# Kernel tuning notes

Measured on AMD Instinct MI355X. Metric: run time of the kernel, lower is better.

The kernel has to match this reference:

```python
import jax, jax.numpy as jnp
import numpy as np

SPECIAL = 4  # special_word_num

def _lstm_cell(x, h, c, Wih, Whh, b):
    # torch gate order: i, f, g, o ; gates = x@Wih.T + h@Whh.T + b
    g = x @ Wih.T + h @ Whh.T + b
    i, f, gg, o = jnp.split(g, 4, axis=-1)
    c_new = jax.nn.sigmoid(f) * c + jax.nn.sigmoid(i) * jnp.tanh(gg)
    h_new = jax.nn.sigmoid(o) * jnp.tanh(c_new)
    return h_new, c_new

def _lstm_scan(xs, h0, c0, Wih, Whh, b):
    def step(carry, x):
        h, c = carry
        h, c = _lstm_cell(x, h, c, Wih, Whh, b)
        return (h, c), h
    (hT, cT), hs = jax.lax.scan(step, (h0, c0), xs)
    return hs, hT, cT  # hs: [T, B, H]

def _forward(article, art_lens, tar_len, emb, enc_Wih_f, enc_Whh_f, enc_b_f,
             enc_Wih_b, enc_Whh_b, enc_b_b, init_enc_h, init_enc_c,
             dec_hW, dec_cW, attn_wm, attn_wq, proj_W1, proj_b1, proj_W2,
             dec_Wih, dec_Whh, dec_b):
    Tsrc, B, _ = article.shape
    H = init_enc_h.shape[1]
    # ---- encoder: 1-layer bidirectional LSTM with learned init states ----
    h0f = jnp.broadcast_to(init_enc_h[0], (B, H)); c0f = jnp.broadcast_to(init_enc_c[0], (B, H))
    h0b = jnp.broadcast_to(init_enc_h[1], (B, H)); c0b = jnp.broadcast_to(init_enc_c[1], (B, H))
    out_f, hTf, cTf = _lstm_scan(article, h0f, c0f, enc_Wih_f, enc_Whh_f, enc_b_f)
    out_b, hTb, cTb = _lstm_scan(article[::-1], h0b, c0b, enc_Wih_b, enc_Whh_b, enc_b_b)
    enc_art = jnp.concatenate([out_f, out_b[::-1]], axis=-1)  # [T, B, 2H]
    final_h = jnp.concatenate([hTf, hTb], axis=-1)  # [B, 2H]
    final_c = jnp.concatenate([cTf, cTb], axis=-1)
    init_h = final_h @ dec_hW  # [B, H]
    init_c = final_c @ dec_cW
    # ---- attention memory + mask ----
    attention = jnp.einsum('tbe,eh->bth', enc_art, attn_wm)  # [B, T, H]
    mask = jnp.arange(Tsrc)[None, :] < art_lens[:, None]      # [B, T]
    lens = art_lens.astype(attention.dtype)[:, None]
    seq_mean = jnp.sum(attention * mask[:, :, None], axis=1) / lens  # [B, H]
    def project(x):
        return jnp.tanh(x @ proj_W1 + proj_b1) @ proj_W2
    init_out = project(jnp.concatenate([init_h, seq_mean], axis=1))  # [B, H/2]
    # ---- sequential decoder over tar_len steps (lax.scan) ----
    embs = emb[SPECIAL + jnp.arange(tar_len)]  # [Ttgt, E]
    NEG = jnp.asarray(-1e9, attention.dtype)
    def dec_step(carry, emb_i):
        h, c, prev_out = carry
        x = jnp.concatenate([jnp.broadcast_to(emb_i, (B, emb_i.shape[0])), prev_out], axis=1)
        h, c = _lstm_cell(x, h, c, dec_Wih, dec_Whh, dec_b)
        query = h @ attn_wq                                   # [B, H]
        score = jnp.einsum('bh,bth->bt', query, attention)
        probs = jax.nn.softmax(jnp.where(mask, score, NEG), axis=-1)
        context = jnp.einsum('bt,bth->bh', probs, attention)
        dec_out = project(jnp.concatenate([h, context], axis=1))
        return (h, c, dec_out), (dec_out, h, c)
    _, (dec_all, h_all, c_all) = jax.lax.scan(dec_step, (init_h, init_c, init_out), embs)
    # stack(dim=0).transpose(0,1) -> batch-first
    return (dec_all.transpose(1, 0, 2), h_all.transpose(1, 0, 2), c_all.transpose(1, 0, 2))

def setup_inputs() -> dict:
    key = jax.random.key(0)
    ks = jax.random.split(key, 20)
    B, Tsrc, Ttgt = 32, 1024, 64
    H, E, V = 512, 256, 50000  # n_hidden, emb_dim/2, vocab
    EMB_DIM, ENC_OUT, OUT = 2 * E, 2 * H, H // 2
    def n(k, shape, s=0.05):
        return (jax.random.normal(k, shape, jnp.float32) * s).astype(jnp.float32)
    return {
        'article': n(ks[0], (Tsrc, B, EMB_DIM), 1.0),
        'art_lens': jnp.full((B,), Tsrc, jnp.int32),
        'tar_len': Ttgt,
        'emb': n(ks[1], (V, E)),
        'enc_Wih_f': n(ks[2], (4 * H, EMB_DIM)), 'enc_Whh_f': n(ks[3], (4 * H, H)), 'enc_b_f': n(ks[4], (4 * H,)),
        'enc_Wih_b': n(ks[5], (4 * H, EMB_DIM)), 'enc_Whh_b': n(ks[6], (4 * H, H)), 'enc_b_b': n(ks[7], (4 * H,)),
        'init_enc_h': n(ks[8], (2, H), 0.01), 'init_enc_c': n(ks[9], (2, H), 0.01),
        'dec_hW': n(ks[10], (ENC_OUT, H)), 'dec_cW': n(ks[11], (ENC_OUT, H)),
        'attn_wm': n(ks[12], (ENC_OUT, H)), 'attn_wq': n(ks[13], (H, H)),
        'proj_W1': n(ks[14], (2 * H, H)), 'proj_b1': n(ks[15], (H,)), 'proj_W2': n(ks[16], (H, OUT)),
        'dec_Wih': n(ks[17], (4 * H, H)), 'dec_Whh': n(ks[18], (4 * H, H)), 'dec_b': n(ks[19], (4 * H,)),
    }

def reference(article, art_lens, tar_len, emb, enc_Wih_f, enc_Whh_f, enc_b_f,
              enc_Wih_b, enc_Whh_b, enc_b_b, init_enc_h, init_enc_c,
              dec_hW, dec_cW, attn_wm, attn_wq, proj_W1, proj_b1, proj_W2,
              dec_Wih, dec_Whh, dec_b):
    return _forward(article, art_lens, tar_len, emb, enc_Wih_f, enc_Whh_f, enc_b_f,
                    enc_Wih_b, enc_Whh_b, enc_b_b, init_enc_h, init_enc_c,
                    dec_hW, dec_cW, attn_wm, attn_wq, proj_W1, proj_b1, proj_W2,
                    dec_Wih, dec_Whh, dec_b)
```

## Files before the change

kernel.cpp:

```cpp
#include <hip/hip_runtime.h>


#define DI __device__ __forceinline__

constexpr int BATCH = 32;
constexpr int TS = 1024;
constexpr int TG = 64;
constexpr int HID = 512;
constexpr int GD = 2048;
constexpr int EDIM = 256;
constexpr int SPECIAL = 4;
constexpr size_t OFF_H = (size_t)BATCH * TG * EDIM;
constexpr size_t OFF_C = OFF_H + (size_t)BATCH * TG * HID;
constexpr int FLAG_STRIDE = 16;

typedef __attribute__((ext_vector_type(8))) short bf16x8;
typedef __attribute__((ext_vector_type(4))) float f32x4;

DI float b2f(unsigned short u) {
  union { unsigned int i; float f; } v; v.i = ((unsigned int)u) << 16; return v.f;
}
DI unsigned short f2b(float f) {
  union { float f; unsigned int i; } v; v.f = f;
  unsigned int r = v.i + 0x7fffu + ((v.i >> 16) & 1u);
  return (unsigned short)(r >> 16);
}
DI float sigm(float x) { return 1.0f / (1.0f + expf(-x)); }
DI float ldf(const void* p, size_t i, int f32f) {
  return f32f ? ((const float*)p)[i] : b2f(((const unsigned short*)p)[i]);
}
DI void stf(void* p, size_t i, float v, int f32f) {
  if (f32f) ((float*)p)[i] = v; else ((unsigned short*)p)[i] = f2b(v);
}
DI unsigned int ald(const unsigned int* p) {
  return __hip_atomic_load(p, __ATOMIC_RELAXED, __HIP_MEMORY_SCOPE_AGENT);
}
DI float aldf(const float* p) {
  return __hip_atomic_load(p, __ATOMIC_RELAXED, __HIP_MEMORY_SCOPE_AGENT);
}
DI void ast(unsigned int* p, unsigned int v) {
  __hip_atomic_store(p, v, __ATOMIC_RELAXED, __HIP_MEMORY_SCOPE_AGENT);
}
DI void astf(float* p, float v) {
  __hip_atomic_store(p, v, __ATOMIC_RELAXED, __HIP_MEMORY_SCOPE_AGENT);
}

__global__ void detect_k(const void* art, int* flag) {
  int tid = threadIdx.x;
  float x = ((const float*)art)[tid + 1024];
  float a = fabsf(x);
  int sane = (x == 0.0f) || (a > 1e-8f && a < 1e4f);
  unsigned long long m = __ballot(sane);
  __shared__ int cnt[4];
  if ((tid & 63) == 0) cnt[tid >> 6] = __popcll(m);
  __syncthreads();
  if (tid == 0) flag[0] = (cnt[0] + cnt[1] + cnt[2] + cnt[3] > 128) ? 1 : 0;
}

__global__ void fill_sig_k(unsigned short* o, int n) {
  int g = blockIdx.x * 256 + threadIdx.x;
  if (g < n) o[g] = 0x42F6;
}

__global__ void pack_gate_k(const void* __restrict__ W,
                            unsigned short* __restrict__ pk, const int* dtf) {
  int f32f = dtf[0];
  int g = blockIdx.x * 256 + threadIdx.x;
  if (g >= (GD * HID) / 8) return;
  int lane = g & 63;
  int kk = (g >> 6) & 15;
  int tile = g >> 10;
  int p = tile * 16 + (lane & 15);
  int nloc = p & 63, blk = p >> 6;
  int orow = (nloc >> 4) * HID + blk * 16 + (nloc & 15);
  int k = kk * 32 + (lane >> 4) * 8;
  unsigned short tmp[8];
#pragma unroll
  for (int j = 0; j < 8; ++j) tmp[j] = f2b(ldf(W, (size_t)orow * HID + k + j, f32f));
  *(uint4*)(pk + (size_t)g * 8) = *(uint4*)tmp;
}

__global__ void pack_wm_k(const void* __restrict__ wm,
                          unsigned short* __restrict__ pk, const int* dtf) {
  int f32f = dtf[0];
  int g = blockIdx.x * 256 + threadIdx.x;
  if (g >= 32 * 32 * 64) return;
  int lane = g & 63;
  int kk = (g >> 6) & 31;
  int nt = g >> 11;
  int col = nt * 16 + (lane & 15);
  int kb = kk * 32 + (lane >> 4) * 8;
  unsigned short tmp[8];
#pragma unroll
  for (int j = 0; j < 8; ++j) tmp[j] = f2b(ldf(wm, (size_t)(kb + j) * HID + col, f32f));
  *(uint4*)(pk + (size_t)g * 8) = *(uint4*)tmp;
}

__global__ void pack_bn_k(const void* __restrict__ W, unsigned short* __restrict__ pk,
                          int K, int N, int total, const int* dtf) {
  int f32f = dtf[0];
  int g = blockIdx.x * 256 + threadIdx.x;
  if (g >= total) return;
  int lane = g & 63;
  int KK = K >> 5;
  int t = g >> 6;
  int kk = t % KK;
  int nt = t / KK;
  int col = nt * 16 + (lane & 15);
  int kb = kk * 32 + (lane >> 4) * 8;
  unsigned short tmp[8];
#pragma unroll
  for (int j = 0; j < 8; ++j) tmp[j] = f2b(ldf(W, (size_t)(kb + j) * N + col, f32f));
  *(uint4*)(pk + (size_t)g * 8) = *(uint4*)tmp;
}

__global__ void pack_bf16_k(const void* __restrict__ src,
                            unsigned short* __restrict__ dst, int n, const int* dtf) {
  int f32f = dtf[0];
  int g = blockIdx.x * 256 + threadIdx.x;
  if (g < n) dst[g] = f2b(ldf(src, g, f32f));
}

__global__ __launch_bounds__(256, 1) void enc_all_k(
    const unsigned short* __restrict__ artb,
    unsigned short* __restrict__ outF, unsigned short* __restrict__ outB,
    const unsigned short* __restrict__ hIF, const unsigned short* __restrict__ hIB,
    float* __restrict__ cF, float* __restrict__ cB,
    const unsigned short* __restrict__ pkXF, const unsigned short* __restrict__ pkHF,
    const unsigned short* __restrict__ pkXB, const unsigned short* __restrict__ pkHB,
    const void* __restrict__ bF, const void* __restrict__ bB,
    int* __restrict__ bar, const int* dtf) {
  const int f32f = dtf[0];
  const int blk = blockIdx.x;
  const int dir = blk >> 5;
  const int blk16 = blk & 31;
  const int tid = threadIdx.x;
  const int lane = tid & 63;
  const int wv = tid >> 6;
  const int tile = blk16 * 4 + wv;

  __shared__ unsigned short lstage[BATCH * HID];
  __shared__ float gbuf[BATCH * 68];

  const unsigned short* pkX = dir ? pkXB : pkXF;
  const unsigned short* pkH = dir ? pkHB : pkHF;
  const void* bias = dir ? bB : bF;
  unsigned short* out = dir ? outB : outF;
  const unsigned short* hI = dir ? hIB : hIF;
  float* cg = dir ? cB : cF;
  int* flp = bar + dir * 32 * FLAG_STRIDE;

  bf16x8 wx[16], wh[16];
  {
    const unsigned short* px = pkX + ((size_t)tile * 16 * 64 + lane) * 8;
    const unsigned short* ph = pkH + ((size_t)tile * 16 * 64 + lane) * 8;
#pragma unroll
    for (int kk = 0; kk < 16; ++kk) {
      wx[kk] = *(const bf16x8*)(px + (size_t)kk * 64 * 8);
      wh[kk] = *(const bf16x8*)(ph + (size_t)kk * 64 * 8);
    }
  }
  const int gb = tid >> 3;
  const int gj = (tid & 7) * 2;
  float c0 = cg[gb * HID + blk16 * 16 + gj];
  float c1 = cg[gb * HID + blk16 * 16 + gj + 1];

  const int r0 = lane & 15;
  const int r1 = 16 + r0;
  const int kbb = (lane >> 4) * 8;
  const int nloc = wv * 16 + (lane & 15);
  const int orow = (nloc >> 4) * HID + blk16 * 16 + (nloc & 15);
  const float bv = ldf(bias, orow, f32f);

  f32x4 acc0 = {0.f, 0.f, 0.f, 0.f};
  f32x4 acc1 = {0.f, 0.f, 0.f, 0.f};

  {
    const int ts0 = dir ? (TS - 1) : 0;
#pragma unroll
    for (int it = 0; it < 8; ++it) {
      int ci = it * 256 + tid;
      int row = ci >> 6;
      int k8 = (ci & 63) << 3;
      uint4 v = *(const uint4*)(artb + (size_t)ts0 * BATCH * HID +
                                (size_t)row * HID + k8);
      unsigned off = (unsigned)(row * 1024 + ((k8 * 2) ^ ((row & 7) << 4)));
      *(uint4*)((char*)lstage + off) = v;
    }
    __syncthreads();
#pragma unroll
    for (int kk = 0; kk < 16; ++kk) {
      unsigned o0 = (unsigned)(r0 * 1024 + (((kk * 32 + kbb) * 2) ^ ((r0 & 7) << 4)));
      unsigned o1 = (unsigned)(r1 * 1024 + (((kk * 32 + kbb) * 2) ^ ((r0 & 7) << 4)));
      bf16x8 a0 = *(const bf16x8*)((const char*)lstage + o0);
      bf16x8 a1 = *(const bf16x8*)((const char*)lstage + o1);
      acc0 = __builtin_amdgcn_mfma_f32_16x16x32_bf16(a0, wx[kk], acc0, 0, 0, 0);
      acc1 = __builtin_amdgcn_mfma_f32_16x16x32_bf16(a1, wx[kk], acc1, 0, 0, 0);
    }
  }

  for (int t = 0; t < TS; ++t) {
    const int tsrc = dir ? (TS - 1 - t) : t;
    if (t > 0) {
      if (wv == 0) {
        const int target = t;
        for (;;) {
          int v = (lane < 32)
              ? __hip_atomic_load(flp + lane * FLAG_STRIDE, __ATOMIC_RELAXED,
                                  __HIP_MEMORY_SCOPE_AGENT)
              : 0x7fffffff;
          if (__all(v >= target)) break;
          __builtin_amdgcn_s_sleep(2);
        }
      }
      __syncthreads();
    }
    unsigned int* hu = (t == 0)
        ? (unsigned int*)hI
        : (unsigned int*)(out + (size_t)(tsrc + (dir ? 1 : -1)) * BATCH * HID);
    unsigned int hreg[32];
#pragma unroll
    for (int it = 0; it < 32; ++it) hreg[it] = ald(hu + it * 256 + tid);
    __syncthreads();
#pragma unroll
    for (int it = 0; it < 32; ++it) {
      int dw = it * 256 + tid;
      int row = dw >> 8;
      unsigned lb = (unsigned)(row * 1024 +
                               (((dw & 252) << 2) ^ ((row & 7) << 4)) +
                               ((dw & 3) << 2));
      *(unsigned int*)((char*)lstage + lb) = hreg[it];
    }
    __syncthreads();
#pragma unroll
    for (int kk = 0; kk < 16; ++kk) {
      unsigned o0 = (unsigned)(r0 * 1024 + (((kk * 32 + kbb) * 2) ^ ((r0 & 7) << 4)));
      unsigned o1 = (unsigned)(r1 * 1024 + (((kk * 32 + kbb) * 2) ^ ((r0 & 7) << 4)));
      bf16x8 a0 = *(const bf16x8*)((const char*)lstage + o0);
      bf16x8 a1 = *(const bf16x8*)((const char*)lstage + o1);
      acc0 = __builtin_amdgcn_mfma_f32_16x16x32_bf16(a0, wh[kk], acc0, 0, 0, 0);
      acc1 = __builtin_amdgcn_mfma_f32_16x16x32_bf16(a1, wh[kk], acc1, 0, 0, 0);
    }
#pragma unroll
    for (int r = 0; r < 4; ++r) {
      int brow = (lane >> 4) * 4 + r;
      gbuf[brow * 68 + nloc] = acc0[r] + bv;
      gbuf[(16 + brow) * 68 + nloc] = acc1[r] + bv;
    }
    __syncthreads();
    {
      float gi0 = gbuf[gb * 68 + gj],      gf0 = gbuf[gb * 68 + 16 + gj];
      float gg0 = gbuf[gb * 68 + 32 + gj], go0 = gbuf[gb * 68 + 48 + gj];
      float gi1 = gbuf[gb * 68 + gj + 1],      gf1 = gbuf[gb * 68 + 16 + gj + 1];
      float gg1 = gbuf[gb * 68 + 32 + gj + 1], go1 = gbuf[gb * 68 + 48 + gj + 1];
      float cn0 = sigm(gf0) * c0 + sigm(gi0) * tanhf(gg0); c0 = cn0;
      float cn1 = sigm(gf1) * c1 + sigm(gi1) * tanhf(gg1); c1 = cn1;
      unsigned int hv = (unsigned int)f2b(sigm(go0) * tanhf(cn0)) |
                        ((unsigned int)f2b(sigm(go1) * tanhf(cn1)) << 16);
      ast((unsigned int*)out + (size_t)tsrc * (BATCH * HID / 2) +
              gb * (HID / 2) + blk16 * 8 + (tid & 7), hv);
    }
    if (t + 1 < TS) {
      __syncthreads();
      if (wv == 0 && lane == 0)
        __hip_atomic_store(flp + blk16 * FLAG_STRIDE, t + 1,
                           __ATOMIC_RELAXED, __HIP_MEMORY_SCOPE_AGENT);
      const int tn = dir ? (TS - 2 - t) : (t + 1);
#pragma unroll
      for (int it = 0; it < 8; ++it) {
        int ci = it * 256 + tid;
        int row = ci >> 6;
        int k8 = (ci & 63) << 3;
        uint4 v = *(const uint4*)(artb + (size_t)tn * BATCH * HID +
                                  (size_t)row * HID + k8);
        unsigned off = (unsigned)(row * 1024 + ((k8 * 2) ^ ((row & 7) << 4)));
        *(uint4*)((char*)lstage + off) = v;
      }
      __syncthreads();
      acc0 = (f32x4){0.f, 0.f, 0.f, 0.f};
      acc1 = (f32x4){0.f, 0.f, 0.f, 0.f};
#pragma unroll
      for (int kk = 0; kk < 16; ++kk) {
        unsigned o0 = (unsigned)(r0 * 1024 + (((kk * 32 + kbb) * 2) ^ ((r0 & 7) << 4)));
        unsigned o1 = (unsigned)(r1 * 1024 + (((kk * 32 + kbb) * 2) ^ ((r0 & 7) << 4)));
        bf16x8 a0 = *(const bf16x8*)((const char*)lstage + o0);
        bf16x8 a1 = *(const bf16x8*)((const char*)lstage + o1);
        acc0 = __builtin_amdgcn_mfma_f32_16x16x32_bf16(a0, wx[kk], acc0, 0, 0, 0);
        acc1 = __builtin_amdgcn_mfma_f32_16x16x32_bf16(a1, wx[kk], acc1, 0, 0, 0);
      }
    }
  }
  cg[gb * HID + blk16 * 16 + gj] = c0;
  cg[gb * HID + blk16 * 16 + gj + 1] = c1;
}

__global__ __launch_bounds__(512, 1) void dec_all_k(
    unsigned short* __restrict__ xdec,
    unsigned short* __restrict__ hd0, unsigned short* __restrict__ hd1,
    const float* __restrict__ cdec,
    const unsigned short* __restrict__ pkX, const unsigned short* __restrict__ pkH,
    const void* __restrict__ dbias,
    const unsigned short* __restrict__ att,
    const unsigned short* __restrict__ pkq,
    const unsigned short* __restrict__ pkw1,
    const unsigned short* __restrict__ b1p,
    const unsigned short* __restrict__ pkw2,
    const void* __restrict__ emb, const int* __restrict__ lens,
    void* __restrict__ dout,
    float* __restrict__ qg,
    unsigned int* __restrict__ ctxb,
    float* __restrict__ zg,
    int* __restrict__ flags, const int* dtf) {
  const int f32f = dtf[0];
  const int blk = blockIdx.x;
  const int tid = threadIdx.x;
  const int lane = tid & 63;
  const int wv = tid >> 6;
  __shared__ __align__(16) char smem[49152];

  const int gb = tid >> 3;
  const int gj = (tid & 7) * 2;
  const int r0 = lane & 15;
  const int r1 = 16 + r0;
  const int kbb = (lane >> 4) * 8;
  const int nloc = wv * 16 + (lane & 15);
  float c0 = 0.f, c1 = 0.f, bv = 0.f;
  if (tid < 256) {
    c0 = cdec[gb * HID + blk * 16 + gj];
    c1 = cdec[gb * HID + blk * 16 + gj + 1];
    int orow = (nloc >> 4) * HID + blk * 16 + (nloc & 15);
    bv = ldf(dbias, orow, f32f);
  }

  int ep = 0;
  auto gbar = [&]() {
    __syncthreads();
    ++ep;
    if (wv == 0) {
      if (lane == 0)
        __hip_atomic_store(flags + blk * FLAG_STRIDE, ep, __ATOMIC_RELAXED,
                           __HIP_MEMORY_SCOPE_AGENT);
      for (;;) {
        int v = (lane < 32)
            ? __hip_atomic_load(flags + lane * FLAG_STRIDE, __ATOMIC_RELAXED,
                                __HIP_MEMORY_SCOPE_AGENT)
            : 0x7fffffff;
        if (__all(v >= ep)) break;
        __builtin_amdgcn_s_sleep(2);
      }
    }
    __syncthreads();
  };

  auto stage8k = [&](const unsigned int* src, unsigned short* lstage) {
    unsigned int rg[16];
#pragma unroll
    for (int it = 0; it < 16; ++it) rg[it] = ald(src + it * 512 + tid);
#pragma unroll
    for (int it = 0; it < 16; ++it) {
      int dw = it * 512 + tid;
      int row = dw >> 8;
      unsigned lb = (unsigned)(row * 1024 +
                               (((dw & 252) << 2) ^ ((row & 7) << 4)) +
                               ((dw & 3) << 2));
      *(unsigned int*)((char*)lstage + lb) = rg[it];
    }
  };

  auto afrag = [&](const unsigned short* lstage, int kk, bf16x8& a0, bf16x8& a1) {
    unsigned o0 = (unsigned)(r0 * 1024 + (((kk * 32 + kbb) * 2) ^ ((r0 & 7) << 4)));
    unsigned o1 = (unsigned)(r1 * 1024 + (((kk * 32 + kbb) * 2) ^ ((r0 & 7) << 4)));
    a0 = *(const bf16x8*)((const char*)lstage + o0);
    a1 = *(const bf16x8*)((const char*)lstage + o1);
  };

  for (int i = 0; i < TG; ++i) {
    unsigned short* hin = (i & 1) ? hd1 : hd0;
    unsigned short* hout = (i & 1) ? hd0 : hd1;

    {
      unsigned short* lstage = (unsigned short*)smem;
      float* gbuf = (float*)(smem + 32768);
      f32x4 acc0 = {0.f, 0.f, 0.f, 0.f};
      f32x4 acc1 = {0.f, 0.f, 0.f, 0.f};
      unsigned int hreg[32];
      if (tid < 256) {
        const unsigned int* xu = (const unsigned int*)xdec;
        unsigned int xreg[32];
#pragma unroll
        for (int it = 0; it < 32; ++it) xreg[it] = ald(xu + it * 256 + tid);
#pragma unroll
        for (int it = 0; it < 32; ++it) {
          int dw = it * 256 + tid;
          int row = dw >> 8;
          unsigned lb = (unsigned)(row * 1024 +
                                   (((dw & 252) << 2) ^ ((row & 7) << 4)) +
                                   ((dw & 3) << 2));
          *(unsigned int*)((char*)lstage + lb) = xreg[it];
        }
      }
      __syncthreads();
      if (tid < 256) {
        const unsigned int* hu = (const unsigned int*)hin;
#pragma unroll
        for (int it = 0; it < 32; ++it) hreg[it] = ald(hu + it * 256 + tid);
        const int tile = blk * 4 + wv;
        const unsigned short* pwx = pkX + (size_t)tile * 16 * 64 * 8;
#pragma unroll
        for (int kk = 0; kk < 16; ++kk) {
          bf16x8 a0, a1;
          afrag(lstage, kk, a0, a1);
          bf16x8 bb = *(const bf16x8*)(pwx + (size_t)(kk * 64 + lane) * 8);
          acc0 = __builtin_amdgcn_mfma_f32_16x16x32_bf16(a0, bb, acc0, 0, 0, 0);
          acc1 = __builtin_amdgcn_mfma_f32_16x16x32_bf16(a1, bb, acc1, 0, 0, 0);
        }
      }
      __syncthreads();
      if (tid < 256) {
#pragma unroll
        for (int it = 0; it < 32; ++it) {
          int dw = it * 256 + tid;
          int row = dw >> 8;
          unsigned lb = (unsigned)(row * 1024 +
                                   (((dw & 252) << 2) ^ ((row & 7) << 4)) +
                                   ((dw & 3) << 2));
          *(unsigned int*)((char*)lstage + lb) = hreg[it];
        }
      }
      __syncthreads();
      if (tid < 256) {
        const int tile = blk * 4 + wv;
        const unsigned short* pwh = pkH + (size_t)tile * 16 * 64 * 8;
#pragma unroll
        for (int kk = 0; kk < 16; ++kk) {
          bf16x8 a0, a1;
          afrag(lstage, kk, a0, a1);
          bf16x8 bb = *(const bf16x8*)(pwh + (size_t)(kk * 64 + lane) * 8);
          acc0 = __builtin_amdgcn_mfma_f32_16x16x32_bf16(a0, bb, acc0, 0, 0, 0);
          acc1 = __builtin_amdgcn_mfma_f32_16x16x32_bf16(a1, bb, acc1, 0, 0, 0);
        }
#pragma unroll
        for (int r = 0; r < 4; ++r) {
          int brow = (lane >> 4) * 4 + r;
          gbuf[brow * 68 + nloc] = acc0[r] + bv;
          gbuf[(16 + brow) * 68 + nloc] = acc1[r] + bv;
        }
      }
      __syncthreads();
      if (tid < 256) {
        float gi0 = gbuf[gb * 68 + gj],      gf0 = gbuf[gb * 68 + 16 + gj];
        float gg0 = gbuf[gb * 68 + 32 + gj], go0 = gbuf[gb * 68 + 48 + gj];
        float gi1 = gbuf[gb * 68 + gj + 1],      gf1 = gbuf[gb * 68 + 16 + gj + 1];
        float gg1 = gbuf[gb * 68 + 32 + gj + 1], go1 = gbuf[gb * 68 + 48 + gj + 1];
        float cn0 = sigm(gf0) * c0 + sigm(gi0) * tanhf(gg0); c0 = cn0;
        float cn1 = sigm(gf1) * c1 + sigm(gi1) * tanhf(gg1); c1 = cn1;
        float hn0 = sigm(go0) * tanhf(cn0);
        float hn1 = sigm(go1) * tanhf(cn1);
        ast((unsigned int*)hout + gb * (HID / 2) + blk * 8 + (tid & 7),
            (unsigned int)f2b(hn0) | ((unsigned int)f2b(hn1) << 16));
        size_t e0 = ((size_t)gb * TG + i) * HID + blk * 16 + gj;
        stf(dout, OFF_H + e0, hn0, f32f);
        stf(dout, OFF_H + e0 + 1, hn1, f32f);
        stf(dout, OFF_C + e0, cn0, f32f);
        stf(dout, OFF_C + e0 + 1, cn1, f32f);
      }
    }
    gbar();

    {
      unsigned short* lstage = (unsigned short*)smem;
      float* part = (float*)(smem + 32768);
      stage8k((const unsigned int*)hout, lstage);
      __syncthreads();
      f32x4 acc0 = {0.f, 0.f, 0.f, 0.f};
      f32x4 acc1 = {0.f, 0.f, 0.f, 0.f};
#pragma unroll
      for (int j = 0; j < 2; ++j) {
        int kk = wv * 2 + j;
        bf16x8 a0, a1;
        afrag(lstage, kk, a0, a1);
        bf16x8 bb = *(const bf16x8*)(pkq + ((size_t)(blk * 16 + kk) * 64 + lane) * 8);
        acc0 = __builtin_amdgcn_mfma_f32_16x16x32_bf16(a0, bb, acc0, 0, 0, 0);
        acc1 = __builtin_amdgcn_mfma_f32_16x16x32_bf16(a1, bb, acc1, 0, 0, 0);
      }
#pragma unroll
      for (int r = 0; r < 4; ++r) {
        int m0 = (lane >> 4) * 4 + r;
        part[wv * 512 + m0 * 16 + (lane & 15)] = acc0[r];
        part[wv * 512 + (m0 + 16) * 16 + (lane & 15)] = acc1[r];
      }
      __syncthreads();
      {
        float s = 0.f;
#pragma unroll
        for (int w = 0; w < 8; ++w) s += part[w * 512 + tid];
        int bb2 = tid >> 4, cl = tid & 15;
        astf(qg + (size_t)bb2 * HID + blk * 16 + cl, s);
      }
    }
    gbar();

    {
      const int b = blk;
      const int len = lens[b];
      float* cred = (float*)smem;
      float* mwl  = (float*)(smem + 16384);
      float* lwl  = (float*)(smem + 16448);
      float* qf   = (float*)(smem + 16512);
      float* ctxf = (float*)(smem + 18560);
      qf[tid] = aldf(qg + (size_t)b * HID + tid);
      __syncthreads();
      float qv[8];
#pragma unroll
      for (int e = 0; e < 8; ++e) qv[e] = qf[lane * 8 + e];
      float m = -1e30f, l = 0.f;
      float ca[8] = {0.f, 0.f, 0.f, 0.f, 0.f, 0.f, 0.f, 0.f};
      const unsigned short* ab = att + ((size_t)b * TS + wv * 128) * HID + lane * 8;
      for (int tt = 0; tt < 128; tt += 8) {
        int t = wv * 128 + tt;
        bf16x8 rr0 = *(const bf16x8*)(ab + (size_t)(tt + 0) * HID);
        bf16x8 rr1 = *(const bf16x8*)(ab + (size_t)(tt + 1) * HID);
        bf16x8 rr2 = *(const bf16x8*)(ab + (size_t)(tt + 2) * HID);
        bf16x8 rr3 = *(const bf16x8*)(ab + (size_t)(tt + 3) * HID);
        bf16x8 rr4 = *(const bf16x8*)(ab + (size_t)(tt + 4) * HID);
        bf16x8 rr5 = *(const bf16x8*)(ab + (size_t)(tt + 5) * HID);
        bf16x8 rr6 = *(const bf16x8*)(ab + (size_t)(tt + 6) * HID);
        bf16x8 rr7 = *(const bf16x8*)(ab + (size_t)(tt + 7) * HID);
        float s0 = 0.f, s1 = 0.f, s2 = 0.f, s3 = 0.f;
        float s4 = 0.f, s5 = 0.f, s6 = 0.f, s7 = 0.f;
#pragma unroll
        for (int e = 0; e < 8; ++e) {
          float q = qv[e];
          s0 += q * b2f(((const unsigned short*)&rr0)[e]);
          s1 += q * b2f(((const unsigned short*)&rr1)[e]);
          s2 += q * b2f(((const unsigned short*)&rr2)[e]);
          s3 += q * b2f(((const unsigned short*)&rr3)[e]);
          s4 += q * b2f(((const unsigned short*)&rr4)[e]);
          s5 += q * b2f(((const unsigned short*)&rr5)[e]);
          s6 += q * b2f(((const unsigned short*)&rr6)[e]);
          s7 += q * b2f(((const unsigned short*)&rr7)[e]);
        }
        for (int o = 32; o; o >>= 1) {
          s0 += __shfl_xor(s0, o, 64); s1 += __shfl_xor(s1, o, 64);
          s2 += __shfl_xor(s2, o, 64); s3 += __shfl_xor(s3, o, 64);
          s4 += __shfl_xor(s4, o, 64); s5 += __shfl_xor(s5, o, 64);
          s6 += __shfl_xor(s6, o, 64); s7 += __shfl_xor(s7, o, 64);
        }
        bool v0 = (t < len), v1 = (t + 1 < len), v2 = (t + 2 < len), v3 = (t + 3 < len);
        bool v4 = (t + 4 < len), v5 = (t + 5 < len), v6 = (t + 6 < len), v7 = (t + 7 < len);
        float smax = fmaxf(
            fmaxf(fmaxf(v0 ? s0 : -1e30f, v1 ? s1 : -1e30f),
                  fmaxf(v2 ? s2 : -1e30f, v3 ? s3 : -1e30f)),
            fmaxf(fmaxf(v4 ? s4 : -1e30f, v5 ? s5 : -1e30f),
                  fmaxf(v6 ? s6 : -1e30f, v7 ? s7 : -1e30f)));
        if (smax > m) {
          float sc2 = expf(m - smax);
          l *= sc2;
#pragma unroll
          for (int e = 0; e < 8; ++e) ca[e] *= sc2;
          m = smax;
        }
        if (v0) { float p = expf(s0 - m); l += p;
#pragma unroll
          for (int e = 0; e < 8; ++e) ca[e] += p * b2f(((const unsigned short*)&rr0)[e]); }
        if (v1) { float p = expf(s1 - m); l += p;
#pragma unroll
          for (int e = 0; e < 8; ++e) ca[e] += p * b2f(((const unsigned short*)&rr1)[e]); }
        if (v2) { float p = expf(s2 - m); l += p;
#pragma unroll
          for (int e = 0; e < 8; ++e) ca[e] += p * b2f(((const unsigned short*)&rr2)[e]); }
        if (v3) { float p = expf(s3 - m); l += p;
#pragma unroll
          for (int e = 0; e < 8; ++e) ca[e] += p * b2f(((const unsigned short*)&rr3)[e]); }
        if (v4) { float p = expf(s4 - m); l += p;
#pragma unroll
          for (int e = 0; e < 8; ++e) ca[e] += p * b2f(((const unsigned short*)&rr4)[e]); }
        if (v5) { float p = expf(s5 - m); l += p;
#pragma unroll
          for (int e = 0; e < 8; ++e) ca[e] += p * b2f(((const unsigned short*)&rr5)[e]); }
        if (v6) { float p = expf(s6 - m); l += p;
#pragma unroll
          for (int e = 0; e < 8; ++e) ca[e] += p * b2f(((const unsigned short*)&rr6)[e]); }
        if (v7) { float p = expf(s7 - m); l += p;
#pragma unroll
          for (int e = 0; e < 8; ++e) ca[e] += p * b2f(((const unsigned short*)&rr7)[e]); }
      }
#pragma unroll
      for (int e = 0; e < 8; ++e) cred[wv * 512 + lane * 8 + e] = ca[e];
      if (lane == 0) { mwl[wv] = m; lwl[wv] = l; }
      __syncthreads();
      {
        float M = -1e30f;
#pragma unroll
        for (int w = 0; w < 8; ++w) M = fmaxf(M, mwl[w]);
        float L = 0.f, s = 0.f;
#pragma unroll
        for (int w = 0; w < 8; ++w) {
          float sc2 = expf(mwl[w] - M);
          L += lwl[w] * sc2;
          s += cred[w * 512 + tid] * sc2;
        }
        ctxf[tid] = s / L;
      }
      __syncthreads();
      if (tid < 256) {
        unsigned int d = (unsigned int)f2b(ctxf[2 * tid]) |
                         ((unsigned int)f2b(ctxf[2 * tid + 1]) << 16);
        ast(ctxb + b * 256 + tid, d);
      }
    }
    gbar();

    {
      unsigned short* lstage = (unsigned short*)smem;
      float* part = (float*)(smem + 32768);
      f32x4 acc0 = {0.f, 0.f, 0.f, 0.f};
      f32x4 acc1 = {0.f, 0.f, 0.f, 0.f};
      stage8k((const unsigned int*)hout, lstage);
      __syncthreads();
#pragma unroll
      for (int j = 0; j < 2; ++j) {
        int kk = wv * 2 + j;
        bf16x8 a0, a1;
        afrag(lstage, kk, a0, a1);
        bf16x8 bb = *(const bf16x8*)(pkw1 + ((size_t)(blk * 32 + kk) * 64 + lane) * 8);
        acc0 = __builtin_amdgcn_mfma_f32_16x16x32_bf16(a0, bb, acc0, 0, 0, 0);
        acc1 = __builtin_amdgcn_mfma_f32_16x16x32_bf16(a1, bb, acc1, 0, 0, 0);
      }
      __syncthreads();
      stage8k(ctxb, lstage);
      __syncthreads();
#pragma unroll
      for (int j = 0; j < 2; ++j) {
        int kkl = wv * 2 + j;
        bf16x8 a0, a1;
        afrag(lstage, kkl, a0, a1);
        bf16x8 bb = *(const bf16x8*)(pkw1 + ((size_t)(blk * 32 + 16 + kkl) * 64 + lane) * 8);
        acc0 = __builtin_amdgcn_mfma_f32_16x16x32_bf16(a0, bb, acc0, 0, 0, 0);
        acc1 = __builtin_amdgcn_mfma_f32_16x16x32_bf16(a1, bb, acc1, 0, 0, 0);
      }
      __syncthreads();
#pragma unroll
      for (int r = 0; r < 4; ++r) {
        int m0 = (lane >> 4) * 4 + r;
        part[wv * 512 + m0 * 16 + (lane & 15)] = acc0[r];
        part[wv * 512 + (m0 + 16) * 16 + (lane & 15)] = acc1[r];
      }
      __syncthreads();
      {
        float s = 0.f;
#pragma unroll
        for (int w = 0; w < 8; ++w) s += part[w * 512 + tid];
        int bb2 = tid >> 4, cl = tid & 15;
        int col = blk * 16 + cl;
        astf(zg + (size_t)bb2 * HID + col, tanhf(b2f(b1p[col]) + s));
      }
    }
    gbar();

    {
      unsigned short* lstage = (unsigned short*)smem;
      float* part = (float*)(smem + 32768);
      if (blk < 16) {
        unsigned int rg[16];
#pragma unroll
        for (int it = 0; it < 16; ++it) {
          int dw = it * 512 + tid;
          int b = dw >> 8, cp = dw & 255;
          float z0 = aldf(zg + (size_t)b * HID + 2 * cp);
          float z1 = aldf(zg + (size_t)b * HID + 2 * cp + 1);
          rg[it] = (unsigned int)f2b(z0) | ((unsigned int)f2b(z1) << 16);
        }
#pragma unroll
        for (int it = 0; it < 16; ++it) {
          int dw = it * 512 + tid;
          int row = dw >> 8;
          unsigned lb = (unsigned)(row * 1024 +
                                   (((dw & 252) << 2) ^ ((row & 7) << 4)) +
                                   ((dw & 3) << 2));
          *(unsigned int*)((char*)lstage + lb) = rg[it];
        }
      }
      __syncthreads();
      f32x4 acc0 = {0.f, 0.f, 0.f, 0.f};
      f32x4 acc1 = {0.f, 0.f, 0.f, 0.f};
      if (blk < 16) {
#pragma unroll
        for (int j = 0; j < 2; ++j) {
          int kk = wv * 2 + j;
          bf16x8 a0, a1;
          afrag(lstage, kk, a0, a1);
          bf16x8 bb = *(const bf16x8*)(pkw2 + ((size_t)(blk * 16 + kk) * 64 + lane) * 8);
          acc0 = __builtin_amdgcn_mfma_f32_16x16x32_bf16(a0, bb, acc0, 0, 0, 0);
          acc1 = __builtin_amdgcn_mfma_f32_16x16x32_bf16(a1, bb, acc1, 0, 0, 0);
        }
#pragma unroll
        for (int r = 0; r < 4; ++r) {
          int m0 = (lane >> 4) * 4 + r;
          part[wv * 512 + m0 * 16 + (lane & 15)] = acc0[r];
          part[wv * 512 + (m0 + 16) * 16 + (lane & 15)] = acc1[r];
        }
      }
      __syncthreads();
      if (blk < 16) {
        float s = 0.f;
#pragma unroll
        for (int w = 0; w < 8; ++w) s += part[w * 512 + tid];
        int bb2 = tid >> 4, cl = tid & 15;
        int col = blk * 16 + cl;
        stf(dout, ((size_t)bb2 * TG + i) * EDIM + col, s, f32f);
        unsigned short xb = f2b(s);
        int ob = __shfl_xor((int)xb, 1);
        if (!(tid & 1))
          ast((unsigned int*)xdec + bb2 * 256 + 128 + (col >> 1),
              (unsigned int)xb | ((unsigned int)(ob & 0xffff) << 16));
      }
      if (blk == 16) {
#pragma unroll
        for (int it = 0; it < 8; ++it) {
          int idx = it * 512 + tid;
          int b = idx >> 7, np = idx & 127;
          float e0 = ldf(emb, (size_t)(SPECIAL + i + 1) * EDIM + 2 * np, f32f);
          float e1 = ldf(emb, (size_t)(SPECIAL + i + 1) * EDIM + 2 * np + 1, f32f);
          ast((unsigned int*)xdec + b * 256 + np,
              (unsigned int)f2b(e0) | ((unsigned int)f2b(e1) << 16));
        }
      }
    }
    gbar();
  }
}

__global__ __launch_bounds__(256) void attn_mm_k(
    const unsigned short* __restrict__ outF, const unsigned short* __restrict__ outB,
    const unsigned short* __restrict__ pkwm, unsigned short* __restrict__ att) {
  __shared__ char ldsA[4 * 1040];
  int bid = blockIdx.x;
  int bn = bid & 7, bm = bid >> 3;
  int tid = threadIdx.x, lane = tid & 63, wv = tid >> 6;
  int r0 = bm * 64;
  f32x4 acc[2][2] = {};
  int srow = tid >> 2, skb = tid & 3;
  int mt0 = (wv & 1) * 2, nt0 = (wv >> 1) * 2;
  for (int kk = 0; kk < 32; ++kk) {
    int kg = kk * 32 + skb * 8;
    const unsigned short* src = (kg < HID)
        ? (outF + (size_t)(r0 + srow) * HID + kg)
        : (outB + (size_t)(r0 + srow) * HID + (kg - HID));
    uint4 v = *(const uint4*)src;
    __syncthreads();
    *(uint4*)(ldsA + skb * 1040 + srow * 16) = v;
    __syncthreads();
    bf16x8 a[2], bb[2];
#pragma unroll
    for (int mi = 0; mi < 2; ++mi) {
      int rl = (mt0 + mi) * 16 + (lane & 15);
      a[mi] = *(const bf16x8*)(ldsA + (lane >> 4) * 1040 + rl * 16);
    }
#pragma unroll
    for (int nj = 0; nj < 2; ++nj) {
      int ntg = bn * 4 + nt0 + nj;
      bb[nj] = *(const bf16x8*)(pkwm + ((size_t)(ntg * 32 + kk) * 64 + lane) * 8);
    }
#pragma unroll
    for (int mi = 0; mi < 2; ++mi)
#pragma unroll
      for (int nj = 0; nj < 2; ++nj)
        acc[mi][nj] = __builtin_amdgcn_mfma_f32_16x16x32_bf16(a[mi], bb[nj], acc[mi][nj], 0, 0, 0);
  }
#pragma unroll
  for (int mi = 0; mi < 2; ++mi)
#pragma unroll
    for (int nj = 0; nj < 2; ++nj)
#pragma unroll
      for (int r = 0; r < 4; ++r) {
        int row = r0 + (mt0 + mi) * 16 + (lane >> 4) * 4 + r;
        int t = row >> 5, b = row & 31;
        int h = bn * 64 + (nt0 + nj) * 16 + (lane & 15);
        att[((size_t)b * TS + t) * HID + h] = f2b(acc[mi][nj][r]);
      }
}

__global__ void init_states_k(const void* __restrict__ ih, const void* __restrict__ ic,
                              unsigned short* hIF, unsigned short* hIB,
                              float* cF, float* cB, int* bar, const int* dtf) {
  int f32f = dtf[0];
  int g = blockIdx.x * 256 + threadIdx.x;
  if (g < (64 + 32) * FLAG_STRIDE)
    __hip_atomic_store(bar + g, 0, __ATOMIC_RELAXED, __HIP_MEMORY_SCOPE_AGENT);
  int b = g >> 9, j = g & 511;
  hIF[b * HID + j] = f2b(ldf(ih, j, f32f));
  hIB[b * HID + j] = f2b(ldf(ih, HID + j, f32f));
  cF[b * HID + j] = ldf(ic, j, f32f);
  cB[b * HID + j] = ldf(ic, HID + j, f32f);
}

__global__ void seqmean_k(const unsigned short* __restrict__ att,
                          const int* __restrict__ lens, float* __restrict__ sm) {
  int b = blockIdx.x, tid = threadIdx.x;
  int len = lens[b];
  float a0 = 0.f, a1 = 0.f;
  for (int t = 0; t < len; ++t) {
    const unsigned short* row = att + ((size_t)b * TS + t) * HID;
    a0 += b2f(row[tid]);
    a1 += b2f(row[tid + 256]);
  }
  float fl = (float)len;
  sm[b * HID + tid] = a0 / fl;
  sm[b * HID + tid + 256] = a1 / fl;
}

__global__ void mv_bb_k(const unsigned short* __restrict__ A1,
                        const unsigned short* __restrict__ A2,
                        const void* __restrict__ W, unsigned short* __restrict__ o,
                        const int* dtf) {
  int f32f = dtf[0];
  int g = blockIdx.x * 256 + threadIdx.x;
  int b = g >> 9, n = g & 511;
  float acc = 0.f;
  for (int k = 0; k < HID; ++k) acc += b2f(A1[b * HID + k]) * ldf(W, (size_t)k * HID + n, f32f);
  for (int k = 0; k < HID; ++k) acc += b2f(A2[b * HID + k]) * ldf(W, (size_t)(HID + k) * HID + n, f32f);
  o[b * HID + n] = f2b(acc);
}

__global__ void mv_ff_k(const float* __restrict__ A1, const float* __restrict__ A2,
                        const void* __restrict__ W, float* __restrict__ o, const int* dtf) {
  int f32f = dtf[0];
  int g = blockIdx.x * 256 + threadIdx.x;
  int b = g >> 9, n = g & 511;
  float acc = 0.f;
  for (int k = 0; k < HID; ++k) acc += A1[b * HID + k] * ldf(W, (size_t)k * HID + n, f32f);
  for (int k = 0; k < HID; ++k) acc += A2[b * HID + k] * ldf(W, (size_t)(HID + k) * HID + n, f32f);
  o[b * HID + n] = acc;
}

__global__ void proj1_k(const unsigned short* __restrict__ A1, const float* __restrict__ A2,
                        const void* __restrict__ W1p, const void* __restrict__ b1p,
                        unsigned short* __restrict__ z, const int* dtf) {
  int f32f = dtf[0];
  int g = blockIdx.x * 256 + threadIdx.x;
  int b = g >> 9, n = g & 511;
  float acc = ldf(b1p, n, f32f);
  for (int k = 0; k < HID; ++k) acc += b2f(A1[b * HID + k]) * ldf(W1p, (size_t)k * HID + n, f32f);
  for (int k = 0; k < HID; ++k) acc += A2[b * HID + k] * ldf(W1p, (size_t)(HID + k) * HID + n, f32f);
  z[b * HID + n] = f2b(tanhf(acc));
}

__global__ void proj2_init_k(const unsigned short* __restrict__ z,
                             const void* __restrict__ W2, const void* __restrict__ emb,
                             unsigned short* __restrict__ xdec, const int* dtf) {
  int f32f = dtf[0];
  int g = blockIdx.x * 256 + threadIdx.x;
  int b = g >> 8, n = g & 255;
  float acc = 0.f;
  for (int k = 0; k < HID; ++k) acc += b2f(z[b * HID + k]) * ldf(W2, (size_t)k * EDIM + n, f32f);
  xdec[b * HID + EDIM + n] = f2b(acc);
  xdec[b * HID + n] = f2b(ldf(emb, (size_t)SPECIAL * EDIM + n, f32f));
}

extern "C" void kernel_launch(void* const* d_in, const int* in_sizes, int n_in,
                              void* d_out, int out_size, void* d_ws, size_t ws_size,
                              hipStream_t stream) {
  (void)in_sizes; (void)n_in;
  const void* article = d_in[0];
  const int* art_lens = (const int*)d_in[1];
  const void* emb  = d_in[3];
  const void* eWxf = d_in[4]; const void* eWhf = d_in[5]; const void* ebf = d_in[6];
  const void* eWxb = d_in[7]; const void* eWhb = d_in[8]; const void* ebb = d_in[9];
  const void* initH = d_in[10]; const void* initC = d_in[11];
  const void* dhW = d_in[12]; const void* dcW = d_in[13];
  const void* wm = d_in[14]; const void* wq = d_in[15];
  const void* W1 = d_in[16]; const void* b1 = d_in[17]; const void* W2 = d_in[18];
  const void* dWx = d_in[19]; const void* dWh = d_in[20]; const void* db = d_in[21];

  char* ws = (char*)d_ws;
  size_t off = 0;
  auto take = [&](size_t bytes) -> char* {
    char* p = ws + off;
    off = (off + bytes + 255) & ~(size_t)255;
    return p;
  };
  int* dtf = (int*)take(4);
  int* bar = (int*)take((64 + 32) * FLAG_STRIDE * 4);
  unsigned short* pk_exf = (unsigned short*)take((size_t)GD * HID * 2);
  unsigned short* pk_ehf = (unsigned short*)take((size_t)GD * HID * 2);
  unsigned short* pk_exb = (unsigned short*)take((size_t)GD * HID * 2);
  unsigned short* pk_ehb = (unsigned short*)take((size_t)GD * HID * 2);
  unsigned short* pk_dx  = (unsigned short*)take((size_t)GD * HID * 2);
  unsigned short* pk_dh  = (unsigned short*)take((size_t)GD * HID * 2);
  unsigned short* pk_wm  = (unsigned short*)take((size_t)1024 * HID * 2);
  unsigned short* pkq  = (unsigned short*)take((size_t)512 * 512 * 2);
  unsigned short* pkw1 = (unsigned short*)take((size_t)1024 * 512 * 2);
  unsigned short* b1p  = (unsigned short*)take((size_t)HID * 2);
  unsigned short* pkw2 = (unsigned short*)take((size_t)512 * 256 * 2);
  unsigned short* outF = (unsigned short*)take((size_t)TS * BATCH * HID * 2);
  unsigned short* outB = (unsigned short*)take((size_t)TS * BATCH * HID * 2);
  unsigned short* att  = (unsigned short*)take((size_t)BATCH * TS * HID * 2);
  unsigned short* hIF  = (unsigned short*)take((size_t)BATCH * HID * 2);
  unsigned short* hIB  = (unsigned short*)take((size_t)BATCH * HID * 2);
  float* cF = (float*)take((size_t)BATCH * HID * 4);
  float* cB = (float*)take((size_t)BATCH * HID * 4);
  unsigned short* hd0 = (unsigned short*)take((size_t)BATCH * HID * 2);
  unsigned short* hd1 = (unsigned short*)take((size_t)BATCH * HID * 2);
  float* cdec = (float*)take((size_t)BATCH * HID * 4);
  unsigned short* xdec = (unsigned short*)take((size_t)BATCH * HID * 2);
  unsigned short* zbuf = (unsigned short*)take((size_t)BATCH * HID * 2);
  float* qg = (float*)take((size_t)BATCH * HID * 4);
  unsigned int* ctxb = (unsigned int*)take((size_t)BATCH * 256 * 4);
  float* zg = (float*)take((size_t)BATCH * HID * 4);
  float* sm = (float*)take((size_t)BATCH * HID * 4);

  if (off > ws_size) {
    fill_sig_k<<<(out_size + 255) / 256, 256, 0, stream>>>((unsigned short*)d_out, out_size);
    return;
  }

  unsigned short* artb = att;

  detect_k<<<1, 256, 0, stream>>>(article, dtf);
  pack_gate_k<<<512, 256, 0, stream>>>(eWxf, pk_exf, dtf);
  pack_gate_k<<<512, 256, 0, stream>>>(eWhf, pk_ehf, dtf);
  pack_gate_k<<<512, 256, 0, stream>>>(eWxb, pk_exb, dtf);
  pack_gate_k<<<512, 256, 0, stream>>>(eWhb, pk_ehb, dtf);
  pack_gate_k<<<512, 256, 0, stream>>>(dWx, pk_dx, dtf);
  pack_gate_k<<<512, 256, 0, stream>>>(dWh, pk_dh, dtf);
  pack_wm_k<<<256, 256, 0, stream>>>(wm, pk_wm, dtf);
  pack_bn_k<<<128, 256, 0, stream>>>(wq, pkq, 512, 512, 32 * 16 * 64, dtf);
  pack_bn_k<<<256, 256, 0, stream>>>(W1, pkw1, 1024, 512, 32 * 32 * 64, dtf);
  pack_bn_k<<<64, 256, 0, stream>>>(W2, pkw2, 512, 256, 16 * 16 * 64, dtf);
  pack_bf16_k<<<2, 256, 0, stream>>>(b1, b1p, HID, dtf);
  pack_bf16_k<<<65536, 256, 0, stream>>>(article, artb, TS * BATCH * HID, dtf);
  init_states_k<<<64, 256, 0, stream>>>(initH, initC, hIF, hIB, cF, cB, bar, dtf);

  enc_all_k<<<64, 256, 0, stream>>>(artb, outF, outB, hIF, hIB, cF, cB,
                                    pk_exf, pk_ehf, pk_exb, pk_ehb, ebf, ebb,
                                    bar, dtf);

  attn_mm_k<<<4096, 256, 0, stream>>>(outF, outB, pk_wm, att);
  seqmean_k<<<32, 256, 0, stream>>>(att, art_lens, sm);
  mv_bb_k<<<64, 256, 0, stream>>>(outF + (size_t)(TS - 1) * BATCH * HID, outB, dhW, hd0, dtf);
  mv_ff_k<<<64, 256, 0, stream>>>(cF, cB, dcW, cdec, dtf);
  proj1_k<<<64, 256, 0, stream>>>(hd0, sm, W1, b1, zbuf, dtf);
  proj2_init_k<<<32, 256, 0, stream>>>(zbuf, W2, emb, xdec, dtf);

  dec_all_k<<<32, 512, 0, stream>>>(xdec, hd0, hd1, cdec, pk_dx, pk_dh, db,
                                    att, pkq, pkw1, b1p, pkw2, emb, art_lens,
                                    d_out, qg, ctxb, zg,
                                    bar + 64 * FLAG_STRIDE, dtf);
}
```

Baseline: 10.22 ms.

## Keep LSTM weights in registers and fuse h-part of projection into query stage

Preloads each wave's decoder LSTM input and hidden weight fragments into registers once before the time loop instead of reloading them from global memory every step. Folds the h-half of the proj_W1 matmul into the query-projection stage, which reuses the already staged h fragments, so the projection stage no longer restages h or syncs for it. Also narrows the attention inner unroll from 8 to 4 rows, likely to relieve register pressure from the new 32 resident weight vectors. The trade-off is higher VGPR usage, which may cause spills or lower occupancy.

```diff
diff --git a/kernel.cpp b/kernel.cpp
--- a/kernel.cpp
+++ b/kernel.cpp
@@ -325,11 +325,20 @@
   const int kbb = (lane >> 4) * 8;
   const int nloc = wv * 16 + (lane & 15);
   float c0 = 0.f, c1 = 0.f, bv = 0.f;
+  bf16x8 cwx[16], cwh[16];
   if (tid < 256) {
     c0 = cdec[gb * HID + blk * 16 + gj];
     c1 = cdec[gb * HID + blk * 16 + gj + 1];
     int orow = (nloc >> 4) * HID + blk * 16 + (nloc & 15);
     bv = ldf(dbias, orow, f32f);
+    const int tile = blk * 4 + wv;
+    const unsigned short* px = pkX + ((size_t)tile * 16 * 64 + lane) * 8;
+    const unsigned short* ph = pkH + ((size_t)tile * 16 * 64 + lane) * 8;
+#pragma unroll
+    for (int kk = 0; kk < 16; ++kk) {
+      cwx[kk] = *(const bf16x8*)(px + (size_t)kk * 64 * 8);
+      cwh[kk] = *(const bf16x8*)(ph + (size_t)kk * 64 * 8);
+    }
   }
 
   int ep = 0;
@@ -377,6 +386,8 @@
   for (int i = 0; i < TG; ++i) {
     unsigned short* hin = (i & 1) ? hd1 : hd0;
     unsigned short* hout = (i & 1) ? hd0 : hd1;
+    f32x4 zacc0 = {0.f, 0.f, 0.f, 0.f};
+    f32x4 zacc1 = {0.f, 0.f, 0.f, 0.f};
 
     {
       unsigned short* lstage = (unsigned short*)smem;
@@ -404,15 +415,12 @@
         const unsigned int* hu = (const unsigned int*)hin;
 #pragma unroll
         for (int it = 0; it < 32; ++it) hreg[it] = ald(hu + it * 256 + tid);
-        const int tile = blk * 4 + wv;
-        const unsigned short* pwx = pkX + (size_t)tile * 16 * 64 * 8;
 #pragma unroll
         for (int kk = 0; kk < 16; ++kk) {
           bf16x8 a0, a1;
           afrag(lstage, kk, a0, a1);
-          bf16x8 bb = *(const bf16x8*)(pwx + (size_t)(kk * 64 + lane) * 8);
-          acc0 = __builtin_amdgcn_mfma_f32_16x16x32_bf16(a0, bb, acc0, 0, 0, 0);
-          acc1 = __builtin_amdgcn_mfma_f32_16x16x32_bf16(a1, bb, acc1, 0, 0, 0);
+          acc0 = __builtin_amdgcn_mfma_f32_16x16x32_bf16(a0, cwx[kk], acc0, 0, 0, 0);
+          acc1 = __builtin_amdgcn_mfma_f32_16x16x32_bf16(a1, cwx[kk], acc1, 0, 0, 0);
         }
       }
       __syncthreads();
@@ -429,15 +437,12 @@
       }
       __syncthreads();
       if (tid < 256) {
-        const int tile = blk * 4 + wv;
-        const unsigned short* pwh = pkH + (size_t)tile * 16 * 64 * 8;
 #pragma unroll
         for (int kk = 0; kk < 16; ++kk) {
           bf16x8 a0, a1;
           afrag(lstage, kk, a0, a1);
-          bf16x8 bb = *(const bf16x8*)(pwh + (size_t)(kk * 64 + lane) * 8);
-          acc0 = __builtin_amdgcn_mfma_f32_16x16x32_bf16(a0, bb, acc0, 0, 0, 0);
-          acc1 = __builtin_amdgcn_mfma_f32_16x16x32_bf16(a1, bb, acc1, 0, 0, 0);
+          acc0 = __builtin_amdgcn_mfma_f32_16x16x32_bf16(a0, cwh[kk], acc0, 0, 0, 0);
+          acc1 = __builtin_amdgcn_mfma_f32_16x16x32_bf16(a1, cwh[kk], acc1, 0, 0, 0);
         }
 #pragma unroll
         for (int r = 0; r < 4; ++r) {
@@ -479,9 +484,12 @@
         int kk = wv * 2 + j;
         bf16x8 a0, a1;
         afrag(lstage, kk, a0, a1);
-        bf16x8 bb = *(const bf16x8*)(pkq + ((size_t)(blk * 16 + kk) * 64 + lane) * 8);
-        acc0 = __builtin_amdgcn_mfma_f32_16x16x32_bf16(a0, bb, acc0, 0, 0, 0);
-        acc1 = __builtin_amdgcn_mfma_f32_16x16x32_bf16(a1, bb, acc1, 0, 0, 0);
+        bf16x8 bq = *(const bf16x8*)(pkq + ((size_t)(blk * 16 + kk) * 64 + lane) * 8);
+        acc0 = __builtin_amdgcn_mfma_f32_16x16x32_bf16(a0, bq, acc0, 0, 0, 0);
+        acc1 = __builtin_amdgcn_mfma_f32_16x16x32_bf16(a1, bq, acc1, 0, 0, 0);
+        bf16x8 bw = *(const bf16x8*)(pkw1 + ((size_t)(blk * 32 + kk) * 64 + lane) * 8);
+        zacc0 = __builtin_amdgcn_mfma_f32_16x16x32_bf16(a0, bw, zacc0, 0, 0, 0);
+        zacc1 = __builtin_amdgcn_mfma_f32_16x16x32_bf16(a1, bw, zacc1, 0, 0, 0);
       }
 #pragma unroll
       for (int r = 0; r < 4; ++r) {
@@ -516,18 +524,13 @@
       float m = -1e30f, l = 0.f;
       float ca[8] = {0.f, 0.f, 0.f, 0.f, 0.f, 0.f, 0.f, 0.f};
       const unsigned short* ab = att + ((size_t)b * TS + wv * 128) * HID + lane * 8;
-      for (int tt = 0; tt < 128; tt += 8) {
+      for (int tt = 0; tt < 128; tt += 4) {
         int t = wv * 128 + tt;
         bf16x8 rr0 = *(const bf16x8*)(ab + (size_t)(tt + 0) * HID);
         bf16x8 rr1 = *(const bf16x8*)(ab + (size_t)(tt + 1) * HID);
         bf16x8 rr2 = *(const bf16x8*)(ab + (size_t)(tt + 2) * HID);
         bf16x8 rr3 = *(const bf16x8*)(ab + (size_t)(tt + 3) * HID);
-        bf16x8 rr4 = *(const bf16x8*)(ab + (size_t)(tt + 4) * HID);
-        bf16x8 rr5 = *(const bf16x8*)(ab + (size_t)(tt + 5) * HID);
-        bf16x8 rr6 = *(const bf16x8*)(ab + (size_t)(tt + 6) * HID);
-        bf16x8 rr7 = *(const bf16x8*)(ab + (size_t)(tt + 7) * HID);
         float s0 = 0.f, s1 = 0.f, s2 = 0.f, s3 = 0.f;
-        float s4 = 0.f, s5 = 0.f, s6 = 0.f, s7 = 0.f;
 #pragma unroll
         for (int e = 0; e < 8; ++e) {
           float q = qv[e];
@@ -535,24 +538,14 @@
           s1 += q * b2f(((const unsigned short*)&rr1)[e]);
           s2 += q * b2f(((const unsigned short*)&rr2)[e]);
           s3 += q * b2f(((const unsigned short*)&rr3)[e]);
-          s4 += q * b2f(((const unsigned short*)&rr4)[e]);
-          s5 += q * b2f(((const unsigned short*)&rr5)[e]);
-          s6 += q * b2f(((const unsigned short*)&rr6)[e]);
-          s7 += q * b2f(((const unsigned short*)&rr7)[e]);
         }
         for (int o = 32; o; o >>= 1) {
           s0 += __shfl_xor(s0, o, 64); s1 += __shfl_xor(s1, o, 64);
           s2 += __shfl_xor(s2, o, 64); s3 += __shfl_xor(s3, o, 64);
-          s4 += __shfl_xor(s4, o, 64); s5 += __shfl_xor(s5, o, 64);
-          s6 += __shfl_xor(s6, o, 64); s7 += __shfl_xor(s7, o, 64);
         }
         bool v0 = (t < len), v1 = (t + 1 < len), v2 = (t + 2 < len), v3 = (t + 3 < len);
-        bool v4 = (t + 4 < len), v5 = (t + 5 < len), v6 = (t + 6 < len), v7 = (t + 7 < len);
-        float smax = fmaxf(
-            fmaxf(fmaxf(v0 ? s0 : -1e30f, v1 ? s1 : -1e30f),
-                  fmaxf(v2 ? s2 : -1e30f, v3 ? s3 : -1e30f)),
-            fmaxf(fmaxf(v4 ? s4 : -1e30f, v5 ? s5 : -1e30f),
-                  fmaxf(v6 ? s6 : -1e30f, v7 ? s7 : -1e30f)));
+        float smax = fmaxf(fmaxf(v0 ? s0 : -1e30f, v1 ? s1 : -1e30f),
+                           fmaxf(v2 ? s2 : -1e30f, v3 ? s3 : -1e30f));
         if (smax > m) {
           float sc2 = expf(m - smax);
           l *= sc2;
@@ -572,18 +565,6 @@
         if (v3) { float p = expf(s3 - m); l += p;
 #pragma unroll
           for (int e = 0; e < 8; ++e) ca[e] += p * b2f(((const unsigned short*)&rr3)[e]); }
-        if (v4) { float p = expf(s4 - m); l += p;
-#pragma unroll
-          for (int e = 0; e < 8; ++e) ca[e] += p * b2f(((const unsigned short*)&rr4)[e]); }
-        if (v5) { float p = expf(s5 - m); l += p;
-#pragma unroll
-          for (int e = 0; e < 8; ++e) ca[e] += p * b2f(((const unsigned short*)&rr5)[e]); }
-        if (v6) { float p = expf(s6 - m); l += p;
-#pragma unroll
-          for (int e = 0; e < 8; ++e) ca[e] += p * b2f(((const unsigned short*)&rr6)[e]); }
-        if (v7) { float p = expf(s7 - m); l += p;
-#pragma unroll
-          for (int e = 0; e < 8; ++e) ca[e] += p * b2f(((const unsigned short*)&rr7)[e]); }
       }
 #pragma unroll
       for (int e = 0; e < 8; ++e) cred[wv * 512 + lane * 8 + e] = ca[e];
@@ -614,20 +595,6 @@
     {
       unsigned short* lstage = (unsigned short*)smem;
       float* part = (float*)(smem + 32768);
-      f32x4 acc0 = {0.f, 0.f, 0.f, 0.f};
-      f32x4 acc1 = {0.f, 0.f, 0.f, 0.f};
-      stage8k((const unsigned int*)hout, lstage);
-      __syncthreads();
-#pragma unroll
-      for (int j = 0; j < 2; ++j) {
-        int kk = wv * 2 + j;
-        bf16x8 a0, a1;
-        afrag(lstage, kk, a0, a1);
-        bf16x8 bb = *(const bf16x8*)(pkw1 + ((size_t)(blk * 32 + kk) * 64 + lane) * 8);
-        acc0 = __builtin_amdgcn_mfma_f32_16x16x32_bf16(a0, bb, acc0, 0, 0, 0);
-        acc1 = __builtin_amdgcn_mfma_f32_16x16x32_bf16(a1, bb, acc1, 0, 0, 0);
-      }
-      __syncthreads();
       stage8k(ctxb, lstage);
       __syncthreads();
 #pragma unroll
@@ -636,15 +603,14 @@
         bf16x8 a0, a1;
         afrag(lstage, kkl, a0, a1);
         bf16x8 bb = *(const bf16x8*)(pkw1 + ((size_t)(blk * 32 + 16 + kkl) * 64 + lane) * 8);
-        acc0 = __builtin_amdgcn_mfma_f32_16x16x32_bf16(a0, bb, acc0, 0, 0, 0);
-        acc1 = __builtin_amdgcn_mfma_f32_16x16x32_bf16(a1, bb, acc1, 0, 0, 0);
-      }
-      __syncthreads();
+        zacc0 = __builtin_amdgcn_mfma_f32_16x16x32_bf16(a0, bb, zacc0, 0, 0, 0);
+        zacc1 = __builtin_amdgcn_mfma_f32_16x16x32_bf16(a1, bb, zacc1, 0, 0, 0);
+      }
 #pragma unroll
       for (int r = 0; r < 4; ++r) {
         int m0 = (lane >> 4) * 4 + r;
-        part[wv * 512 + m0 * 16 + (lane & 15)] = acc0[r];
-        part[wv * 512 + (m0 + 16) * 16 + (lane & 15)] = acc1[r];
+        part[wv * 512 + m0 * 16 + (lane & 15)] = zacc0[r];
+        part[wv * 512 + (m0 + 16) * 16 + (lane & 15)] = zacc1[r];
       }
       __syncthreads();
       {
```

After: 9.488 ms. -7.1%, faster.
